# Kernel optimization log

Hardware: AMD Instinct MI355X
Metric: run time of the kernel (lower is better)

## Reference

```python
import jax, jax.numpy as jnp
import numpy as np

S, D_IN, D_OUT = 4096, 1024, 1024

def setup_inputs() -> dict:
    key = jax.random.key(0)
    kx, kq, kk, kv = jax.random.split(key, 4)
    scale = 0.02
    return {
        "x": jax.random.normal(kx, (S, D_IN), dtype=jnp.float32),
        "W_query": jax.random.normal(kq, (D_IN, D_OUT), dtype=jnp.float32) * scale,
        "W_key": jax.random.normal(kk, (D_IN, D_OUT), dtype=jnp.float32) * scale,
        "W_value": jax.random.normal(kv, (D_IN, D_OUT), dtype=jnp.float32) * scale,
    }

def reference(x, W_query, W_key, W_value):
    # x: [S, d_in]; W_*: [d_in, d_out]
    queries = x @ W_query        # [S, d_out]
    keys = x @ W_key             # [S, d_out]
    values = x @ W_value         # [S, d_out]
    d_k = keys.shape[-1]
    attn_scores = queries @ keys.T            # [S, S]
    attn_weights = jax.nn.softmax(attn_scores / jnp.sqrt(jnp.float32(d_k)), axis=-1)
    context_vec = attn_weights @ values       # [S, d_out]
    return context_vec
```

## Files before the change

### kernel.cpp

```cpp
#include <hip/hip_runtime.h>

typedef _Float16 f16x8 __attribute__((ext_vector_type(8)));
typedef float f32x4 __attribute__((ext_vector_type(4)));
typedef unsigned short u16;
typedef u16 u16x8 __attribute__((ext_vector_type(8)));
typedef u16 u16x4 __attribute__((ext_vector_type(4)));

__device__ __forceinline__ u16 f2h_bits(float f) {
    _Float16 h = (_Float16)f;
    return __builtin_bit_cast(u16, h);
}
__device__ __forceinline__ float h2f(u16 b) {
    return (float)__builtin_bit_cast(_Float16, b);
}

typedef __attribute__((address_space(1))) unsigned int gu32_as1;
typedef __attribute__((address_space(3))) unsigned int lu32_as3;
__device__ __forceinline__ void gload16(const u16* g, u16* l) {
    __builtin_amdgcn_global_load_lds((gu32_as1*)g, (lu32_as3*)l, 16, 0, 0);
}

template <int MODE>
__global__ __launch_bounds__(256, 4) void gemm_bt(
    const u16* __restrict__ A, int lda,
    const u16* __restrict__ B, int ldb,
    u16* __restrict__ C, int ldc,
    int Ksplit, float alpha, size_t c_z_stride,
    int bnW, int bmW, int numPanelX,
    float* __restrict__ rowsum, u16* __restrict__ vt)
{
    __shared__ __attribute__((aligned(16))) u16 As[8192];
    __shared__ __attribute__((aligned(16))) u16 Bs[8192];

    const int t    = threadIdx.x;
    const int lane = t & 63;
    const int wave = t >> 6;
    const int wm   = wave & 1;
    const int wn   = wave >> 1;
    const int l16  = lane & 15;
    const int quad = lane >> 4;

    const int lin = blockIdx.y * gridDim.x + blockIdx.x;
    const int xcd = lin & 7;
    const int idx = lin >> 3;
    const int px  = xcd % numPanelX;
    const int py  = xcd / numPanelX;
    const int bn  = px * bnW + idx % bnW;
    const int bm  = py * bmW + idx / bnW;

    const int kz = blockIdx.z;
    A += (size_t)kz * Ksplit;
    B += (size_t)kz * Ksplit;
    C += (size_t)kz * c_z_stride;

    const int srow = t >> 2;
    const int scol = ((t & 3) ^ ((t >> 3) & 3)) * 8;

    const u16* Ag = A + (size_t)(bm * 128 + srow) * lda + scol;
    const u16* Bg = B + (size_t)(bn * 128 + srow) * ldb + scol;
    const size_t a64 = (size_t)64 * lda;
    const size_t b64 = (size_t)64 * ldb;

    u16* AsD = &As[t * 8];
    u16* BsD = &Bs[t * 8];

#define STAGE(bufv, k0) do {                                     \
        gload16(Ag + (k0),       AsD + (bufv) * 4096);           \
        gload16(Ag + (k0) + a64, AsD + (bufv) * 4096 + 2048);    \
        gload16(Bg + (k0),       BsD + (bufv) * 4096);           \
        gload16(Bg + (k0) + b64, BsD + (bufv) * 4096 + 2048);    \
    } while (0)

    const int fseg = (quad ^ ((l16 >> 1) & 3)) * 8;
    const u16* Afr = &As[(wm * 64 + l16) * 32 + fseg];
    const u16* Bfr = &Bs[(wn * 64 + l16) * 32 + fseg];

    f32x4 acc[4][4] = {};

    const int NT = Ksplit >> 5;

    STAGE(0, 0);

    for (int k = 0; k < NT; ++k) {
        const int cur = k & 1;
        __syncthreads();
        if (k + 1 < NT) STAGE(cur ^ 1, (k + 1) * 32);

        f16x8 af[4], bfv[4];
#pragma unroll
        for (int i = 0; i < 4; i++)
            af[i]  = *(const f16x8*)(Afr + cur * 4096 + i * 512);
#pragma unroll
        for (int i = 0; i < 4; i++)
            bfv[i] = *(const f16x8*)(Bfr + cur * 4096 + i * 512);
#pragma unroll
        for (int mi = 0; mi < 4; mi++)
#pragma unroll
            for (int ni = 0; ni < 4; ni++)
                acc[mi][ni] = __builtin_amdgcn_mfma_f32_16x16x32_f16(
                    af[mi], bfv[ni], acc[mi][ni], 0, 0, 0);
    }
#undef STAGE

    const int crow = bm * 128 + wm * 64 + quad * 4;
    const int ccol = bn * 128 + wn * 64 + l16;

    if (MODE == 1) {
        float rs[4][4];
#pragma unroll
        for (int mi = 0; mi < 4; mi++)
#pragma unroll
            for (int r = 0; r < 4; r++) rs[mi][r] = 0.f;
#pragma unroll
        for (int mi = 0; mi < 4; mi++) {
#pragma unroll
            for (int ni = 0; ni < 4; ni++) {
#pragma unroll
                for (int r = 0; r < 4; r++) {
                    float e = __expf(acc[mi][ni][r] * alpha);
                    rs[mi][r] += e;
                    C[(size_t)(crow + mi * 16 + r) * ldc + (ccol + ni * 16)] = f2h_bits(e);
                }
            }
        }
#pragma unroll
        for (int mi = 0; mi < 4; mi++) {
#pragma unroll
            for (int r = 0; r < 4; r++) {
                float s = rs[mi][r];
#pragma unroll
                for (int o = 1; o < 16; o <<= 1) s += __shfl_xor(s, o);
                if (l16 == 0)
                    atomicAdd(&rowsum[crow + mi * 16 + r], s);
            }
        }
    } else if (MODE == 2 && bn >= 16) {
#pragma unroll
        for (int ni = 0; ni < 4; ni++) {
            const int cV = (bn - 16) * 128 + wn * 64 + ni * 16 + l16;
#pragma unroll
            for (int mi = 0; mi < 4; mi++) {
                u16x4 o;
#pragma unroll
                for (int r = 0; r < 4; r++) o[r] = f2h_bits(acc[mi][ni][r]);
                *(u16x4*)(vt + (size_t)cV * 4096 + crow + mi * 16) = o;
            }
        }
    } else {
#pragma unroll
        for (int mi = 0; mi < 4; mi++)
#pragma unroll
            for (int ni = 0; ni < 4; ni++)
#pragma unroll
                for (int r = 0; r < 4; r++)
                    C[(size_t)(crow + mi * 16 + r) * ldc + (ccol + ni * 16)] =
                        f2h_bits(acc[mi][ni][r] * alpha);
    }
}

__global__ __launch_bounds__(256) void cast_to_f16(
    const float* __restrict__ in, u16* __restrict__ out, int n)
{
    int i = (blockIdx.x * 256 + threadIdx.x) * 4;
    if (i + 3 < n) {
        float4 v = *(const float4*)(in + i);
        ushort4 o;
        o.x = f2h_bits(v.x);
        o.y = f2h_bits(v.y);
        o.z = f2h_bits(v.z);
        o.w = f2h_bits(v.w);
        *(ushort4*)(out + i) = o;
    }
}

__global__ __launch_bounds__(256) void transpose_w3(
    const float* __restrict__ W0, const float* __restrict__ W1,
    const float* __restrict__ W2, u16* __restrict__ out)
{
    const float* in = (blockIdx.z == 0) ? W0 : (blockIdx.z == 1) ? W1 : W2;
    u16* o = out + (size_t)blockIdx.z * 1024 * 1024;
    __shared__ float tile[32][33];
    const int bx = blockIdx.x * 32;
    const int by = blockIdx.y * 32;
    const int tx = threadIdx.x, ty = threadIdx.y;
#pragma unroll
    for (int j = 0; j < 4; j++)
        tile[ty + j * 8][tx] = in[(size_t)(by + ty + j * 8) * 1024 + bx + tx];
    __syncthreads();
#pragma unroll
    for (int j = 0; j < 4; j++)
        o[(size_t)(bx + ty + j * 8) * 1024 + by + tx] = f2h_bits(tile[tx][ty + j * 8]);
}

__global__ __launch_bounds__(256) void zero_f32(float* __restrict__ p, int n)
{
    int i = (blockIdx.x * 256 + threadIdx.x) * 4;
    if (i + 3 < n) *(float4*)(p + i) = float4{0.f, 0.f, 0.f, 0.f};
}

__global__ __launch_bounds__(256) void add_div4(
    const u16* __restrict__ P, const float* __restrict__ l,
    float* __restrict__ o)
{
    const size_t zs = (size_t)4096 * 1024;
    int i = (blockIdx.x * 256 + threadIdx.x) * 8;
    float inv = 1.0f / l[i >> 10];
    float s[8] = {};
#pragma unroll
    for (int z = 0; z < 4; z++) {
        u16x8 h = *(const u16x8*)(P + z * zs + i);
#pragma unroll
        for (int j = 0; j < 8; j++) s[j] += h2f(h[j]);
    }
    float4 lo{s[0] * inv, s[1] * inv, s[2] * inv, s[3] * inv};
    float4 hi{s[4] * inv, s[5] * inv, s[6] * inv, s[7] * inv};
    *(float4*)(o + i) = lo;
    *(float4*)(o + i + 4) = hi;
}

extern "C" void kernel_launch(void* const* d_in, const int* in_sizes, int n_in,
                              void* d_out, int out_size, void* d_ws, size_t ws_size,
                              hipStream_t stream)
{
    (void)in_sizes; (void)n_in; (void)out_size; (void)ws_size;
    const float* x  = (const float*)d_in[0];
    const float* Wq = (const float*)d_in[1];
    const float* Wk = (const float*)d_in[2];
    const float* Wv = (const float*)d_in[3];
    float* out = (float*)d_out;
    char* ws = (char*)d_ws;

    u16* xb  = (u16*)(ws);
    u16* Wt  = (u16*)(ws + ((size_t)8  << 20));
    u16* QK  = (u16*)(ws + ((size_t)14 << 20));
    u16* Sb  = (u16*)(ws + ((size_t)32 << 20));
    u16* Vt  = (u16*)(ws + ((size_t)64 << 20));
    float* lr = (float*)(ws + ((size_t)72 << 20));
    u16* P   = (u16*)(ws);

    const int S = 4096, D = 1024;
    dim3 tb(32, 8);

    cast_to_f16<<<(S * D) / (4 * 256), 256, 0, stream>>>(x, xb, S * D);

    transpose_w3<<<dim3(32, 32, 3), tb, 0, stream>>>(Wq, Wk, Wv, Wt);

    gemm_bt<2><<<dim3(3072 / 128, S / 128, 1), 256, 0, stream>>>(
        xb, D, Wt, D, QK, 2048, D, 1.0f, 0, 6, 16, 4, nullptr, Vt);

    zero_f32<<<S / (4 * 256), 256, 0, stream>>>(lr, S);

    gemm_bt<1><<<dim3(S / 128, S / 128, 1), 256, 0, stream>>>(
        QK, 2048, QK + 1024, 2048, Sb, S, D, 0.03125f, 0, 8, 16, 4, lr, nullptr);

    gemm_bt<0><<<dim3(D / 128, S / 128, 4), 256, 0, stream>>>(
        Sb, S, Vt, S, P, D, 1024, 1.0f, (size_t)S * D, 4, 8, 2, nullptr, nullptr);

    add_div4<<<(S * D) / (8 * 256), 256, 0, stream>>>(P, lr, out);
}
```

Baseline: 224.2 us.

## Enlarge GEMM tiles to 256x256 with 512 threads and 4-stage async pipeline

Each GEMM block now computes a 256x256 tile with 8 waves instead of 128x128 with 4 waves, and each wave holds 8x4 MFMA accumulators. The LDS double buffer becomes a 4-deep ring with three k-tiles prefetched, synchronised by explicit vmcnt waits and raw barriers in place of __syncthreads. The aim is more operand reuse per load and better hiding of global-load latency. In exchange, LDS use grows to 128 KB per block and register pressure rises, which lowers occupancy, and the smaller grids give fewer blocks to spread across CUs.

```diff
diff --git a/kernel.cpp b/kernel.cpp
--- a/kernel.cpp
+++ b/kernel.cpp
@@ -21,7 +21,7 @@
 }
 
 template <int MODE>
-__global__ __launch_bounds__(256, 4) void gemm_bt(
+__global__ __launch_bounds__(512, 2) void gemm_bt(
     const u16* __restrict__ A, int lda,
     const u16* __restrict__ B, int ldb,
     u16* __restrict__ C, int ldc,
@@ -29,14 +29,14 @@
     int bnW, int bmW, int numPanelX,
     float* __restrict__ rowsum, u16* __restrict__ vt)
 {
-    __shared__ __attribute__((aligned(16))) u16 As[8192];
-    __shared__ __attribute__((aligned(16))) u16 Bs[8192];
+    __shared__ __attribute__((aligned(16))) u16 As[32768];
+    __shared__ __attribute__((aligned(16))) u16 Bs[32768];
 
     const int t    = threadIdx.x;
     const int lane = t & 63;
     const int wave = t >> 6;
-    const int wm   = wave & 1;
-    const int wn   = wave >> 1;
+    const int wm   = wave >> 2;
+    const int wn   = wave & 3;
     const int l16  = lane & 15;
     const int quad = lane >> 4;
 
@@ -54,65 +54,81 @@
     C += (size_t)kz * c_z_stride;
 
     const int srow = t >> 2;
-    const int scol = ((t & 3) ^ ((t >> 3) & 3)) * 8;
-
-    const u16* Ag = A + (size_t)(bm * 128 + srow) * lda + scol;
-    const u16* Bg = B + (size_t)(bn * 128 + srow) * ldb + scol;
-    const size_t a64 = (size_t)64 * lda;
-    const size_t b64 = (size_t)64 * ldb;
+    const int sseg = ((t & 3) ^ ((t >> 3) & 3)) * 8;
+
+    const u16* Ag = A + (size_t)(bm * 256 + srow) * lda + sseg;
+    const u16* Bg = B + (size_t)(bn * 256 + srow) * ldb + sseg;
+    const size_t a128 = (size_t)128 * lda;
+    const size_t b128 = (size_t)128 * ldb;
 
     u16* AsD = &As[t * 8];
     u16* BsD = &Bs[t * 8];
 
-#define STAGE(bufv, k0) do {                                     \
-        gload16(Ag + (k0),       AsD + (bufv) * 4096);           \
-        gload16(Ag + (k0) + a64, AsD + (bufv) * 4096 + 2048);    \
-        gload16(Bg + (k0),       BsD + (bufv) * 4096);           \
-        gload16(Bg + (k0) + b64, BsD + (bufv) * 4096 + 2048);    \
+#define STAGE(bufv, kt) do {                                       \
+        const u16* _ga = Ag + (size_t)(kt) * 32;                   \
+        const u16* _gb = Bg + (size_t)(kt) * 32;                   \
+        u16* _la = AsD + (bufv) * 8192;                            \
+        u16* _lb = BsD + (bufv) * 8192;                            \
+        gload16(_ga,        _la);              \
+        gload16(_ga + a128, _la + 4096);       \
+        gload16(_gb,        _lb);              \
+        gload16(_gb + b128, _lb + 4096);       \
     } while (0)
 
-    const int fseg = (quad ^ ((l16 >> 1) & 3)) * 8;
-    const u16* Afr = &As[(wm * 64 + l16) * 32 + fseg];
-    const u16* Bfr = &Bs[(wn * 64 + l16) * 32 + fseg];
-
-    f32x4 acc[4][4] = {};
+    const int fslot = (quad ^ ((l16 >> 1) & 3)) * 8;
+    const u16* Afr = &As[wm * 4096 + l16 * 32 + fslot];
+    const u16* Bfr = &Bs[wn * 2048 + l16 * 32 + fslot];
+
+    f32x4 acc[8][4] = {};
 
     const int NT = Ksplit >> 5;
 
     STAGE(0, 0);
+    STAGE(1, 1);
+    STAGE(2, 2);
+    asm volatile("s_waitcnt vmcnt(8)" ::: "memory");
+    __builtin_amdgcn_s_barrier();
+    asm volatile("" ::: "memory");
 
     for (int k = 0; k < NT; ++k) {
-        const int cur = k & 1;
-        __syncthreads();
-        if (k + 1 < NT) STAGE(cur ^ 1, (k + 1) * 32);
-
-        f16x8 af[4], bfv[4];
-#pragma unroll
-        for (int i = 0; i < 4; i++)
-            af[i]  = *(const f16x8*)(Afr + cur * 4096 + i * 512);
-#pragma unroll
-        for (int i = 0; i < 4; i++)
-            bfv[i] = *(const f16x8*)(Bfr + cur * 4096 + i * 512);
-#pragma unroll
-        for (int mi = 0; mi < 4; mi++)
-#pragma unroll
-            for (int ni = 0; ni < 4; ni++)
-                acc[mi][ni] = __builtin_amdgcn_mfma_f32_16x16x32_f16(
-                    af[mi], bfv[ni], acc[mi][ni], 0, 0, 0);
+        const int buf = k & 3;
+
+        f16x8 af[8], bf[4];
+#pragma unroll
+        for (int mi = 0; mi < 8; mi++)
+            af[mi] = *(const f16x8*)(Afr + buf * 8192 + mi * 512);
+#pragma unroll
+        for (int nj = 0; nj < 4; nj++)
+            bf[nj] = *(const f16x8*)(Bfr + buf * 8192 + nj * 512);
+
+        if (k + 3 < NT) STAGE((k + 3) & 3, k + 3);
+
+#pragma unroll
+        for (int mi = 0; mi < 8; mi++)
+#pragma unroll
+            for (int nj = 0; nj < 4; nj++)
+                acc[mi][nj] = __builtin_amdgcn_mfma_f32_16x16x32_f16(
+                    af[mi], bf[nj], acc[mi][nj], 0, 0, 0);
+
+        if (k < NT - 3)       asm volatile("s_waitcnt vmcnt(8)" ::: "memory");
+        else if (k == NT - 3) asm volatile("s_waitcnt vmcnt(4)" ::: "memory");
+        else if (k == NT - 2) asm volatile("s_waitcnt vmcnt(0)" ::: "memory");
+        __builtin_amdgcn_s_barrier();
+        asm volatile("" ::: "memory");
     }
 #undef STAGE
 
-    const int crow = bm * 128 + wm * 64 + quad * 4;
-    const int ccol = bn * 128 + wn * 64 + l16;
+    const int crow = bm * 256 + wm * 128 + quad * 4;
+    const int ccol = bn * 256 + wn * 64 + l16;
 
     if (MODE == 1) {
-        float rs[4][4];
-#pragma unroll
-        for (int mi = 0; mi < 4; mi++)
+        float rs[8][4];
+#pragma unroll
+        for (int mi = 0; mi < 8; mi++)
 #pragma unroll
             for (int r = 0; r < 4; r++) rs[mi][r] = 0.f;
 #pragma unroll
-        for (int mi = 0; mi < 4; mi++) {
+        for (int mi = 0; mi < 8; mi++) {
 #pragma unroll
             for (int ni = 0; ni < 4; ni++) {
 #pragma unroll
@@ -124,7 +140,7 @@
             }
         }
 #pragma unroll
-        for (int mi = 0; mi < 4; mi++) {
+        for (int mi = 0; mi < 8; mi++) {
 #pragma unroll
             for (int r = 0; r < 4; r++) {
                 float s = rs[mi][r];
@@ -134,12 +150,12 @@
                     atomicAdd(&rowsum[crow + mi * 16 + r], s);
             }
         }
-    } else if (MODE == 2 && bn >= 16) {
+    } else if (MODE == 2 && bn >= 8) {
 #pragma unroll
         for (int ni = 0; ni < 4; ni++) {
-            const int cV = (bn - 16) * 128 + wn * 64 + ni * 16 + l16;
-#pragma unroll
-            for (int mi = 0; mi < 4; mi++) {
+            const int cV = (bn - 8) * 256 + wn * 64 + ni * 16 + l16;
+#pragma unroll
+            for (int mi = 0; mi < 8; mi++) {
                 u16x4 o;
 #pragma unroll
                 for (int r = 0; r < 4; r++) o[r] = f2h_bits(acc[mi][ni][r]);
@@ -148,7 +164,7 @@
         }
     } else {
 #pragma unroll
-        for (int mi = 0; mi < 4; mi++)
+        for (int mi = 0; mi < 8; mi++)
 #pragma unroll
             for (int ni = 0; ni < 4; ni++)
 #pragma unroll
@@ -245,16 +261,16 @@
 
     transpose_w3<<<dim3(32, 32, 3), tb, 0, stream>>>(Wq, Wk, Wv, Wt);
 
-    gemm_bt<2><<<dim3(3072 / 128, S / 128, 1), 256, 0, stream>>>(
-        xb, D, Wt, D, QK, 2048, D, 1.0f, 0, 6, 16, 4, nullptr, Vt);
+    gemm_bt<2><<<dim3(12, 16, 1), 512, 0, stream>>>(
+        xb, D, Wt, D, QK, 2048, D, 1.0f, 0, 3, 8, 4, nullptr, Vt);
 
     zero_f32<<<S / (4 * 256), 256, 0, stream>>>(lr, S);
 
-    gemm_bt<1><<<dim3(S / 128, S / 128, 1), 256, 0, stream>>>(
-        QK, 2048, QK + 1024, 2048, Sb, S, D, 0.03125f, 0, 8, 16, 4, lr, nullptr);
-
-    gemm_bt<0><<<dim3(D / 128, S / 128, 4), 256, 0, stream>>>(
-        Sb, S, Vt, S, P, D, 1024, 1.0f, (size_t)S * D, 4, 8, 2, nullptr, nullptr);
+    gemm_bt<1><<<dim3(16, 16, 1), 512, 0, stream>>>(
+        QK, 2048, QK + 1024, 2048, Sb, S, D, 0.03125f, 0, 4, 8, 4, lr, nullptr);
+
+    gemm_bt<0><<<dim3(4, 16, 4), 512, 0, stream>>>(
+        Sb, S, Vt, S, P, D, 1024, 1.0f, (size_t)S * D, 1, 8, 4, nullptr, nullptr);
 
     add_div4<<<(S * D) / (8 * 256), 256, 0, stream>>>(P, lr, out);
 }
```

Result: faster. 216.4 us (-3.5%).
